# Performance work log

Measured on AMD Instinct MI355X. Metric: run time of the kernel, lower is better.

Reference implementation:

```python
import jax, jax.numpy as jnp
import numpy as np

N = 100000
E = 1600000
D_IN = 128
D_OUT = 128
LN_EPS = 1e-5


def setup_inputs() -> dict:
    key = jax.random.key(0)
    ks = jax.random.split(key, 5)
    features = jax.random.normal(ks[0], (N, D_IN), dtype=jnp.float32)
    adj_indices = jax.random.randint(ks[1], (2, E), 0, N, dtype=jnp.int64)
    adj_values = jax.random.uniform(ks[2], (E,), dtype=jnp.float32)
    weight = jax.random.normal(ks[3], (D_IN, D_OUT), dtype=jnp.float32) * (1.0 / np.sqrt(D_IN))
    bias = jax.random.normal(ks[4], (1, D_OUT), dtype=jnp.float32) * 0.1
    ln_gamma = jnp.ones((D_OUT,), dtype=jnp.float32)
    ln_beta = jnp.zeros((D_OUT,), dtype=jnp.float32)
    return {
        "features": features,
        "adj_indices": adj_indices,
        "adj_values": adj_values,
        "weight": weight,
        "bias": bias,
        "ln_gamma": ln_gamma,
        "ln_beta": ln_beta,
    }


def reference(features, adj_indices, adj_values, weight, bias, ln_gamma, ln_beta):
    # Dense transform: [N, in] @ [in, out] -> [N, out]
    h = features @ weight
    # SpMM: out[r] = sum_{edges (r,c)} val * h[c]
    row, col = adj_indices[0], adj_indices[1]
    msg = adj_values[:, None] * h[col]  # [E, out] gather + scale
    agg = jax.ops.segment_sum(msg, row, num_segments=features.shape[0])
    # bias + ELU
    x = jax.nn.elu(agg + bias)
    # LayerNorm over last dim (eps=1e-5, learned affine)
    mu = jnp.mean(x, axis=-1, keepdims=True)
    var = jnp.mean(jnp.square(x - mu), axis=-1, keepdims=True)
    return (x - mu) * jax.lax.rsqrt(var + LN_EPS) * ln_gamma + ln_beta
```

## Files before the change

kernel.cpp:

```cpp
#include <hip/hip_runtime.h>
#include <hip/hip_bf16.h>

#define LN_EPS 1e-5f

typedef float f32x4 __attribute__((ext_vector_type(4)));
typedef short s16x8 __attribute__((ext_vector_type(8)));

__device__ __forceinline__ unsigned short f2bf(float f) {
  return __builtin_bit_cast(unsigned short, __float2bfloat16(f));
}
__device__ __forceinline__ float bf_lo(unsigned int u) { return __uint_as_float(u << 16); }
__device__ __forceinline__ float bf_hi(unsigned int u) { return __uint_as_float(u & 0xFFFF0000u); }

__global__ __launch_bounds__(512) void k_build(const unsigned int* __restrict__ idx,
                                               const float* __restrict__ vals,
                                               const float* __restrict__ feats,
                                               const float* __restrict__ W,
                                               int E, int N, int CAP, int SB,
                                               int* __restrict__ scnt,
                                               int2* __restrict__ brec,
                                               unsigned int* __restrict__ hu) {
  __shared__ __align__(16) char smem[34816];
  int t = threadIdx.x;
  if ((int)blockIdx.x < SB) {
    int* lcnt = (int*)smem;
    int* lbase = lcnt + 1024;
    int* sflag = lbase + 1024;
    if (t == 0) *sflag = 0;
    for (int i = t; i < 1024; i += 512) lcnt[i] = 0;
    __syncthreads();
    {
      int nchk = E < 4096 ? E : 4096;
      unsigned int orv = 0u;
      for (int i = t; i < nchk; i += 512) orv |= idx[2 * i + 1];
      if (orv) atomicOr(sflag, 1);
    }
    __syncthreads();
    bool is64 = (*sflag == 0);
    int xcd = blockIdx.x & 7;
    int e0 = blockIdx.x * 4096 + t * 8;
    int rows[8], cols[8], lrk[8];
    float vv[8];
    if (e0 + 7 < E) {
      if (is64) {
#pragma unroll
        for (int q = 0; q < 4; ++q) {
          int4 a = *(const int4*)(idx + 2 * e0 + 4 * q);
          rows[2 * q] = a.x; rows[2 * q + 1] = a.z;
          int4 c = *(const int4*)(idx + 2 * E + 2 * e0 + 4 * q);
          cols[2 * q] = c.x; cols[2 * q + 1] = c.z;
        }
      } else {
        const int* p = (const int*)idx;
#pragma unroll
        for (int q = 0; q < 2; ++q) {
          int4 a = *(const int4*)(p + e0 + 4 * q);
          rows[4 * q] = a.x; rows[4 * q + 1] = a.y; rows[4 * q + 2] = a.z; rows[4 * q + 3] = a.w;
          int4 c = *(const int4*)(p + E + e0 + 4 * q);
          cols[4 * q] = c.x; cols[4 * q + 1] = c.y; cols[4 * q + 2] = c.z; cols[4 * q + 3] = c.w;
        }
      }
      float4 va = *(const float4*)(vals + e0);
      float4 vb = *(const float4*)(vals + e0 + 4);
      vv[0] = va.x; vv[1] = va.y; vv[2] = va.z; vv[3] = va.w;
      vv[4] = vb.x; vv[5] = vb.y; vv[6] = vb.z; vv[7] = vb.w;
    } else {
#pragma unroll
      for (int q = 0; q < 8; ++q) {
        int e = e0 + q;
        rows[q] = -1;
        if (e < E) {
          rows[q] = is64 ? (int)idx[2 * e] : ((const int*)idx)[e];
          cols[q] = is64 ? (int)idx[2 * E + 2 * e] : ((const int*)idx)[E + e];
          vv[q] = vals[e];
        }
      }
    }
#pragma unroll
    for (int q = 0; q < 8; ++q)
      if (rows[q] >= 0) lrk[q] = atomicAdd(&lcnt[rows[q] >> 7], 1);
    __syncthreads();
    for (int i = t; i < 1024; i += 512) {
      int c = lcnt[i];
      lbase[i] = c ? atomicAdd(&scnt[(i * 8 + xcd) * 16], c) : 0;
    }
    __syncthreads();
#pragma unroll
    for (int q = 0; q < 8; ++q) {
      if (rows[q] >= 0) {
        int bk = rows[q] >> 7;
        int p = lbase[bk] + lrk[q];
        if (p < CAP)
          brec[(size_t)(bk * 8 + xcd) * CAP + p] =
              make_int2(cols[q] | ((rows[q] & 127) << 20), __float_as_int(vv[q]));
      }
    }
  } else {
    unsigned short (*Wt)[136] = (unsigned short(*)[136])smem;
    for (int i = t; i < 16384; i += 512) {
      int k = i & 127, c = i >> 7;
      Wt[c][k] = f2bf(W[k * 128 + c]);
    }
    __syncthreads();
    int wid = t >> 6, lane = t & 63;
    int rlo = lane & 15, khi = lane >> 4;
    int row0 = (blockIdx.x - SB) * 128 + wid * 16;
    f32x4 zero = {0.f, 0.f, 0.f, 0.f};
    f32x4 acc[8];
#pragma unroll
    for (int n = 0; n < 8; ++n) acc[n] = zero;
#pragma unroll
    for (int kb = 0; kb < 4; ++kb) {
      int k0 = kb * 32 + khi * 8;
      int r = row0 + rlo;
      if (r > N - 1) r = N - 1;
      const float* p = feats + (size_t)r * 128 + k0;
      f32x4 a0 = *(const f32x4*)p;
      f32x4 a1 = *(const f32x4*)(p + 4);
      s16x8 af;
#pragma unroll
      for (int j = 0; j < 4; ++j) af[j] = (short)f2bf(a0[j]);
#pragma unroll
      for (int j = 0; j < 4; ++j) af[4 + j] = (short)f2bf(a1[j]);
#pragma unroll
      for (int n = 0; n < 8; ++n) {
        s16x8 bfr = *(const s16x8*)&Wt[n * 16 + rlo][k0];
        acc[n] = __builtin_amdgcn_mfma_f32_16x16x32_bf16(af, bfr, acc[n], 0, 0, 0);
      }
    }
#pragma unroll
    for (int n = 0; n < 4; ++n)
#pragma unroll
      for (int reg = 0; reg < 4; ++reg) {
        int r = row0 + khi * 4 + reg;
        if (r < N) {
          unsigned int lo = f2bf(acc[n][reg]);
          unsigned int hi = f2bf(acc[n + 4][reg]);
          hu[(size_t)r * 64 + n * 16 + rlo] = lo | (hi << 16);
        }
      }
  }
}

__global__ __launch_bounds__(512) void k_localize(const int* __restrict__ scnt, int CAP,
                                                  const int2* __restrict__ brec, int N,
                                                  int* __restrict__ rowbeg,
                                                  int* __restrict__ rowcnt,
                                                  int2* __restrict__ brec2) {
  __shared__ int pref[9];
  __shared__ int cnt[128], basei[128], cur[128];
  int b = blockIdx.x, t = threadIdx.x;
  if (t < 128) { cnt[t] = 0; cur[t] = 0; }
  if (t == 0) {
    int s = 0;
#pragma unroll
    for (int x = 0; x < 8; ++x) { pref[x] = s; s += min(scnt[(b * 8 + x) * 16], CAP); }
    pref[8] = s;
  }
  __syncthreads();
  for (int x = 0; x < 8; ++x) {
    int sc = pref[x + 1] - pref[x];
    const int2* sp = brec + (size_t)(b * 8 + x) * CAP;
    for (int i = t; i < sc; i += 512) atomicAdd(&cnt[(unsigned)sp[i].x >> 20], 1);
  }
  __syncthreads();
  if (t < 128) basei[t] = cnt[t];
  __syncthreads();
  for (int d = 1; d < 128; d <<= 1) {
    int v = 0;
    if (t < 128 && t >= d) v = basei[t - d];
    __syncthreads();
    if (t < 128) basei[t] += v;
    __syncthreads();
  }
  int bstr = b * 8 * CAP;
  if (t < 128) {
    int r = b * 128 + t;
    if (r < N) { rowbeg[r] = bstr + basei[t] - cnt[t]; rowcnt[r] = cnt[t]; }
  }
  __syncthreads();
  for (int x = 0; x < 8; ++x) {
    int sc = pref[x + 1] - pref[x];
    const int2* sp = brec + (size_t)(b * 8 + x) * CAP;
    for (int i = t; i < sc; i += 512) {
      int2 e = sp[i];
      int lr = (unsigned)e.x >> 20;
      int p = atomicAdd(&cur[lr], 1);
      brec2[bstr + basei[lr] - cnt[lr] + p] = make_int2(e.x & 0xFFFFF, e.y);
    }
  }
}

__global__ __launch_bounds__(256) void k_spmm3(const unsigned int* __restrict__ hu,
                                               const int* __restrict__ rowbeg,
                                               const int* __restrict__ rowcnt,
                                               const int2* __restrict__ rec,
                                               const float* __restrict__ bias,
                                               const float* __restrict__ gamma,
                                               const float* __restrict__ beta,
                                               float* __restrict__ out, int N) {
  int wid = __builtin_amdgcn_readfirstlane(threadIdx.x >> 6);
  int lane = threadIdx.x & 63;
  int r = blockIdx.x * 4 + wid;
  if (r >= N) return;
  int start = rowbeg[r], end = start + rowcnt[r];

  float a0 = 0.f, a1 = 0.f;
  int i = start;
  for (; i + 8 <= end; i += 8) {
    unsigned int u[8];
    float v[8];
#pragma unroll
    for (int j = 0; j < 8; ++j) {
      int2 e = rec[i + j];
      u[j] = hu[(size_t)e.x * 64 + lane];
      v[j] = __int_as_float(e.y);
    }
#pragma unroll
    for (int j = 0; j < 8; ++j) {
      a0 = fmaf(v[j], bf_lo(u[j]), a0);
      a1 = fmaf(v[j], bf_hi(u[j]), a1);
    }
  }
  for (; i + 4 <= end; i += 4) {
    unsigned int u[4];
    float v[4];
#pragma unroll
    for (int j = 0; j < 4; ++j) {
      int2 e = rec[i + j];
      u[j] = hu[(size_t)e.x * 64 + lane];
      v[j] = __int_as_float(e.y);
    }
#pragma unroll
    for (int j = 0; j < 4; ++j) {
      a0 = fmaf(v[j], bf_lo(u[j]), a0);
      a1 = fmaf(v[j], bf_hi(u[j]), a1);
    }
  }
  for (; i < end; ++i) {
    int2 e = rec[i];
    unsigned int u = hu[(size_t)e.x * 64 + lane];
    float v = __int_as_float(e.y);
    a0 = fmaf(v, bf_lo(u), a0);
    a1 = fmaf(v, bf_hi(u), a1);
  }

  float x0 = a0 + bias[lane], x1 = a1 + bias[lane + 64];
  x0 = x0 > 0.f ? x0 : __expf(x0) - 1.f;
  x1 = x1 > 0.f ? x1 : __expf(x1) - 1.f;

  float s = x0 + x1;
#pragma unroll
  for (int d = 1; d < 64; d <<= 1) s += __shfl_xor(s, d);
  float mu = s * (1.f / 128.f);
  float d0 = x0 - mu, d1 = x1 - mu;
  float q = d0 * d0 + d1 * d1;
#pragma unroll
  for (int d = 1; d < 64; d <<= 1) q += __shfl_xor(q, d);
  float rstd = rsqrtf(q * (1.f / 128.f) + LN_EPS);

  float o0 = d0 * rstd * gamma[lane] + beta[lane];
  float o1 = d1 * rstd * gamma[lane + 64] + beta[lane + 64];
  __builtin_nontemporal_store(o0, out + (size_t)r * 128 + lane);
  __builtin_nontemporal_store(o1, out + (size_t)r * 128 + 64 + lane);
}

extern "C" void kernel_launch(void* const* d_in, const int* in_sizes, int n_in,
                              void* d_out, int out_size, void* d_ws, size_t ws_size,
                              hipStream_t stream) {
  const float* feats = (const float*)d_in[0];
  const unsigned int* idx = (const unsigned int*)d_in[1];
  const float* vals = (const float*)d_in[2];
  const float* W = (const float*)d_in[3];
  const float* bias = (const float*)d_in[4];
  const float* gamma = (const float*)d_in[5];
  const float* beta = (const float*)d_in[6];
  float* out = (float*)d_out;
  int N = in_sizes[0] / 128;
  int E = in_sizes[2];
  (void)n_in; (void)out_size; (void)ws_size;

  int NBUK = (N + 127) >> 7;
  int NV = NBUK * 8;
  int mean = (E + NV - 1) / NV;
  int CAP = ((mean + mean / 2 + 15) / 16) * 16;

  char* ws = (char*)d_ws;
  size_t off = 0;
  auto alloc = [&](size_t bytes) {
    char* p = ws + off;
    off += (bytes + 255) & ~(size_t)255;
    return p;
  };
  unsigned int* hu = (unsigned int*)alloc((size_t)N * 64 * 4);
  int* scnt  = (int*)alloc((size_t)NV * 64);
  int* rowbeg = (int*)alloc((size_t)N * 4);
  int* rowcnt = (int*)alloc((size_t)N * 4);
  int2* brec  = (int2*)alloc((size_t)NV * CAP * 8);
  int2* brec2 = (int2*)alloc((size_t)NV * CAP * 8);

  hipMemsetAsync(scnt, 0, (size_t)NV * 64, stream);

  int SB = (E + 4095) / 4096;
  int GEMMB = (N + 127) / 128;
  k_build<<<SB + GEMMB, 512, 0, stream>>>(idx, vals, feats, W, E, N, CAP, SB, scnt, brec, hu);
  k_localize<<<NBUK, 512, 0, stream>>>(scnt, CAP, brec, N, rowbeg, rowcnt, brec2);
  k_spmm3<<<(N + 3) / 4, 256, 0, stream>>>(hu, rowbeg, rowcnt, brec2, bias, gamma, beta, out, N);
}
```

Before: 139.8 us.

## Stage bucket records in LDS for localize, pack row info, widen spmm blocks

Adds a localize variant that loads each bucket's records once into registers, counts them per row, and scatters into shared memory. It then writes the output contiguously, instead of reading the records twice and scattering to global memory. Row start and count are packed into a single int2 array, so the spmm kernel does one load per row. The spmm kernel now uses 512-thread blocks and hoists its bias, gamma and beta loads. The old localize remains as a fallback when the bucket capacity exceeds the shared buffer.

```diff
diff --git a/kernel.cpp b/kernel.cpp
--- a/kernel.cpp
+++ b/kernel.cpp
@@ -142,11 +142,76 @@
   }
 }
 
-__global__ __launch_bounds__(512) void k_localize(const int* __restrict__ scnt, int CAP,
-                                                  const int2* __restrict__ brec, int N,
-                                                  int* __restrict__ rowbeg,
-                                                  int* __restrict__ rowcnt,
-                                                  int2* __restrict__ brec2) {
+#define LCAP 3072
+#define LRPT 6
+__global__ __launch_bounds__(512) void k_localize_s(const int* __restrict__ scnt, int CAP,
+                                                    const int2* __restrict__ brec, int N,
+                                                    int2* __restrict__ rowinfo,
+                                                    int2* __restrict__ brec2) {
+  __shared__ int2 srec[LCAP];
+  __shared__ int cnt[128], base[128], prefs[9];
+  __shared__ int w0sum;
+  int b = blockIdx.x, t = threadIdx.x;
+  if (t < 128) cnt[t] = 0;
+  if (t == 0) {
+    int s = 0;
+#pragma unroll
+    for (int x = 0; x < 8; ++x) { prefs[x] = s; s += min(scnt[(b * 8 + x) * 16], CAP); }
+    prefs[8] = s;
+  }
+  __syncthreads();
+  int pr[9];
+#pragma unroll
+  for (int x = 0; x < 9; ++x) pr[x] = prefs[x];
+  int M = pr[8];
+
+  int2 myrec[LRPT];
+  int lr[LRPT], lrk[LRPT];
+#pragma unroll
+  for (int q = 0; q < LRPT; ++q) {
+    int i = q * 512 + t;
+    lr[q] = -1;
+    if (i < M) {
+      int x = 0;
+#pragma unroll
+      for (int xx = 1; xx < 8; ++xx) x += (i >= pr[xx]) ? 1 : 0;
+      myrec[q] = brec[(size_t)(b * 8 + x) * CAP + (i - pr[x])];
+      lr[q] = (unsigned)myrec[q].x >> 20;
+      lrk[q] = atomicAdd(&cnt[lr[q]], 1);
+    }
+  }
+  __syncthreads();
+  int c = (t < 128) ? cnt[t] : 0;
+  int inc = c;
+#pragma unroll
+  for (int d = 1; d < 64; d <<= 1) {
+    int y = __shfl_up(inc, d);
+    if ((t & 63) >= d) inc += y;
+  }
+  if (t == 63) w0sum = inc;
+  __syncthreads();
+  if (t >= 64 && t < 128) inc += w0sum;
+  if (t < 128) base[t] = inc - c;
+  __syncthreads();
+#pragma unroll
+  for (int q = 0; q < LRPT; ++q)
+    if (lr[q] >= 0) srec[base[lr[q]] + lrk[q]] = myrec[q];
+  int bstr = b * 8 * CAP;
+  if (t < 128) {
+    int r = b * 128 + t;
+    if (r < N) rowinfo[r] = make_int2(bstr + base[t], c);
+  }
+  __syncthreads();
+  for (int i = t; i < M; i += 512) {
+    int2 e = srec[i];
+    brec2[bstr + i] = make_int2(e.x & 0xFFFFF, e.y);
+  }
+}
+
+__global__ __launch_bounds__(512) void k_localize_l(const int* __restrict__ scnt, int CAP,
+                                                    const int2* __restrict__ brec, int N,
+                                                    int2* __restrict__ rowinfo,
+                                                    int2* __restrict__ brec2) {
   __shared__ int pref[9];
   __shared__ int cnt[128], basei[128], cur[128];
   int b = blockIdx.x, t = threadIdx.x;
@@ -176,7 +241,7 @@
   int bstr = b * 8 * CAP;
   if (t < 128) {
     int r = b * 128 + t;
-    if (r < N) { rowbeg[r] = bstr + basei[t] - cnt[t]; rowcnt[r] = cnt[t]; }
+    if (r < N) rowinfo[r] = make_int2(bstr + basei[t] - cnt[t], cnt[t]);
   }
   __syncthreads();
   for (int x = 0; x < 8; ++x) {
@@ -184,16 +249,15 @@
     const int2* sp = brec + (size_t)(b * 8 + x) * CAP;
     for (int i = t; i < sc; i += 512) {
       int2 e = sp[i];
-      int lr = (unsigned)e.x >> 20;
-      int p = atomicAdd(&cur[lr], 1);
-      brec2[bstr + basei[lr] - cnt[lr] + p] = make_int2(e.x & 0xFFFFF, e.y);
-    }
-  }
-}
-
-__global__ __launch_bounds__(256) void k_spmm3(const unsigned int* __restrict__ hu,
-                                               const int* __restrict__ rowbeg,
-                                               const int* __restrict__ rowcnt,
+      int lrr = (unsigned)e.x >> 20;
+      int p = atomicAdd(&cur[lrr], 1);
+      brec2[bstr + basei[lrr] - cnt[lrr] + p] = make_int2(e.x & 0xFFFFF, e.y);
+    }
+  }
+}
+
+__global__ __launch_bounds__(512) void k_spmm3(const unsigned int* __restrict__ hu,
+                                               const int2* __restrict__ rowinfo,
                                                const int2* __restrict__ rec,
                                                const float* __restrict__ bias,
                                                const float* __restrict__ gamma,
@@ -201,9 +265,13 @@
                                                float* __restrict__ out, int N) {
   int wid = __builtin_amdgcn_readfirstlane(threadIdx.x >> 6);
   int lane = threadIdx.x & 63;
-  int r = blockIdx.x * 4 + wid;
+  int r = blockIdx.x * 8 + wid;
   if (r >= N) return;
-  int start = rowbeg[r], end = start + rowcnt[r];
+  float b0 = bias[lane], b1 = bias[lane + 64];
+  float g0 = gamma[lane], g1 = gamma[lane + 64];
+  float be0 = beta[lane], be1 = beta[lane + 64];
+  int2 ri = rowinfo[r];
+  int start = ri.x, end = ri.x + ri.y;
 
   float a0 = 0.f, a1 = 0.f;
   int i = start;
@@ -245,7 +313,7 @@
     a1 = fmaf(v, bf_hi(u), a1);
   }
 
-  float x0 = a0 + bias[lane], x1 = a1 + bias[lane + 64];
+  float x0 = a0 + b0, x1 = a1 + b1;
   x0 = x0 > 0.f ? x0 : __expf(x0) - 1.f;
   x1 = x1 > 0.f ? x1 : __expf(x1) - 1.f;
 
@@ -259,8 +327,8 @@
   for (int d = 1; d < 64; d <<= 1) q += __shfl_xor(q, d);
   float rstd = rsqrtf(q * (1.f / 128.f) + LN_EPS);
 
-  float o0 = d0 * rstd * gamma[lane] + beta[lane];
-  float o1 = d1 * rstd * gamma[lane + 64] + beta[lane + 64];
+  float o0 = d0 * rstd * g0 + be0;
+  float o1 = d1 * rstd * g1 + be1;
   __builtin_nontemporal_store(o0, out + (size_t)r * 128 + lane);
   __builtin_nontemporal_store(o1, out + (size_t)r * 128 + 64 + lane);
 }
@@ -294,8 +362,7 @@
   };
   unsigned int* hu = (unsigned int*)alloc((size_t)N * 64 * 4);
   int* scnt  = (int*)alloc((size_t)NV * 64);
-  int* rowbeg = (int*)alloc((size_t)N * 4);
-  int* rowcnt = (int*)alloc((size_t)N * 4);
+  int2* rowinfo = (int2*)alloc((size_t)N * 8);
   int2* brec  = (int2*)alloc((size_t)NV * CAP * 8);
   int2* brec2 = (int2*)alloc((size_t)NV * CAP * 8);
 
@@ -304,6 +371,9 @@
   int SB = (E + 4095) / 4096;
   int GEMMB = (N + 127) / 128;
   k_build<<<SB + GEMMB, 512, 0, stream>>>(idx, vals, feats, W, E, N, CAP, SB, scnt, brec, hu);
-  k_localize<<<NBUK, 512, 0, stream>>>(scnt, CAP, brec, N, rowbeg, rowcnt, brec2);
-  k_spmm3<<<(N + 3) / 4, 256, 0, stream>>>(hu, rowbeg, rowcnt, brec2, bias, gamma, beta, out, N);
-}
+  if (8 * CAP <= LCAP)
+    k_localize_s<<<NBUK, 512, 0, stream>>>(scnt, CAP, brec, N, rowinfo, brec2);
+  else
+    k_localize_l<<<NBUK, 512, 0, stream>>>(scnt, CAP, brec, N, rowinfo, brec2);
+  k_spmm3<<<(N + 7) / 8, 512, 0, stream>>>(hu, rowinfo, brec2, bias, gamma, beta, out, N);
+}
```

Result: faster. 133.6 us (-4.4%).

## Fuse row localization into SpMM kernel using shared-memory bucket sort

Applied to the files above, without the earlier changes.

Buckets shrink from 128 to 64 rows, and the separate localize kernel is merged into the SpMM kernel. Each block now loads its bucket's edge records, counting-sorts them by local row in LDS, then aggregates and applies bias, ELU and LayerNorm per row. This removes one kernel launch and the global round trip through brec2, rowbeg and rowcnt. In exchange, the per-bucket capacity becomes a mean plus 8-sigma bound clamped to the LDS size, so edges beyond the cap would be silently dropped on skewed graphs. Each block also handles fewer rows with a serial per-warp loop.

```diff
diff --git a/kernel.cpp b/kernel.cpp
--- a/kernel.cpp
+++ b/kernel.cpp
@@ -1,5 +1,6 @@
 #include <hip/hip_runtime.h>
 #include <hip/hip_bf16.h>
+#include <math.h>
 
 #define LN_EPS 1e-5f
 
@@ -11,6 +12,7 @@
 }
 __device__ __forceinline__ float bf_lo(unsigned int u) { return __uint_as_float(u << 16); }
 __device__ __forceinline__ float bf_hi(unsigned int u) { return __uint_as_float(u & 0xFFFF0000u); }
+
 
 __global__ __launch_bounds__(512) void k_build(const unsigned int* __restrict__ idx,
                                                const float* __restrict__ vals,
@@ -24,10 +26,10 @@
   int t = threadIdx.x;
   if ((int)blockIdx.x < SB) {
     int* lcnt = (int*)smem;
-    int* lbase = lcnt + 1024;
-    int* sflag = lbase + 1024;
+    int* lbase = lcnt + 2048;
+    int* sflag = lbase + 2048;
     if (t == 0) *sflag = 0;
-    for (int i = t; i < 1024; i += 512) lcnt[i] = 0;
+    for (int i = t; i < 2048; i += 512) lcnt[i] = 0;
     __syncthreads();
     {
       int nchk = E < 4096 ? E : 4096;
@@ -78,9 +80,9 @@
     }
 #pragma unroll
     for (int q = 0; q < 8; ++q)
-      if (rows[q] >= 0) lrk[q] = atomicAdd(&lcnt[rows[q] >> 7], 1);
-    __syncthreads();
-    for (int i = t; i < 1024; i += 512) {
+      if (rows[q] >= 0) lrk[q] = atomicAdd(&lcnt[rows[q] >> 6], 1);
+    __syncthreads();
+    for (int i = t; i < 2048; i += 512) {
       int c = lcnt[i];
       lbase[i] = c ? atomicAdd(&scnt[(i * 8 + xcd) * 16], c) : 0;
     }
@@ -88,11 +90,11 @@
 #pragma unroll
     for (int q = 0; q < 8; ++q) {
       if (rows[q] >= 0) {
-        int bk = rows[q] >> 7;
+        int bk = rows[q] >> 6;
         int p = lbase[bk] + lrk[q];
         if (p < CAP)
           brec[(size_t)(bk * 8 + xcd) * CAP + p] =
-              make_int2(cols[q] | ((rows[q] & 127) << 20), __float_as_int(vv[q]));
+              make_int2(cols[q] | ((rows[q] & 63) << 20), __float_as_int(vv[q]));
       }
     }
   } else {
@@ -142,127 +144,130 @@
   }
 }
 
-__global__ __launch_bounds__(512) void k_localize(const int* __restrict__ scnt, int CAP,
-                                                  const int2* __restrict__ brec, int N,
-                                                  int* __restrict__ rowbeg,
-                                                  int* __restrict__ rowcnt,
-                                                  int2* __restrict__ brec2) {
-  __shared__ int pref[9];
-  __shared__ int cnt[128], basei[128], cur[128];
+#define SCAPMAX 2048
+#define LRPT 4
+__global__ __launch_bounds__(512, 8) void k_spmmL(const unsigned int* __restrict__ hu,
+                                                  const int* __restrict__ scnt, int CAP,
+                                                  const int2* __restrict__ brec,
+                                                  const float* __restrict__ bias,
+                                                  const float* __restrict__ gamma,
+                                                  const float* __restrict__ beta,
+                                                  float* __restrict__ out, int N) {
+  __shared__ int2 srec[SCAPMAX];
+  __shared__ int cnt[64], base[64], prefs[9];
   int b = blockIdx.x, t = threadIdx.x;
-  if (t < 128) { cnt[t] = 0; cur[t] = 0; }
+  int wid = __builtin_amdgcn_readfirstlane(t >> 6);
+  int lane = t & 63;
+  if (t < 64) cnt[t] = 0;
   if (t == 0) {
     int s = 0;
 #pragma unroll
-    for (int x = 0; x < 8; ++x) { pref[x] = s; s += min(scnt[(b * 8 + x) * 16], CAP); }
-    pref[8] = s;
-  }
+    for (int x = 0; x < 8; ++x) { prefs[x] = s; s += min(scnt[(b * 8 + x) * 16], CAP); }
+    prefs[8] = s;
+  }
+  float b0 = bias[lane], b1 = bias[lane + 64];
+  float g0 = gamma[lane], g1 = gamma[lane + 64];
+  float be0 = beta[lane], be1 = beta[lane + 64];
   __syncthreads();
-  for (int x = 0; x < 8; ++x) {
-    int sc = pref[x + 1] - pref[x];
-    const int2* sp = brec + (size_t)(b * 8 + x) * CAP;
-    for (int i = t; i < sc; i += 512) atomicAdd(&cnt[(unsigned)sp[i].x >> 20], 1);
+  int pr[9];
+#pragma unroll
+  for (int x = 0; x < 9; ++x) pr[x] = prefs[x];
+  int M = pr[8];
+
+  int2 myrec[LRPT];
+  int lr[LRPT], lrk[LRPT];
+#pragma unroll
+  for (int q = 0; q < LRPT; ++q) {
+    int i = q * 512 + t;
+    lr[q] = -1;
+    if (i < M) {
+      int x = 0;
+#pragma unroll
+      for (int xx = 1; xx < 8; ++xx) x += (i >= pr[xx]) ? 1 : 0;
+      myrec[q] = brec[(size_t)(b * 8 + x) * CAP + (i - pr[x])];
+      lr[q] = (unsigned)myrec[q].x >> 20;
+      lrk[q] = atomicAdd(&cnt[lr[q]], 1);
+    }
   }
   __syncthreads();
-  if (t < 128) basei[t] = cnt[t];
+  if (t < 64) {
+    int c = cnt[t];
+    int inc = c;
+#pragma unroll
+    for (int d = 1; d < 64; d <<= 1) {
+      int y = __shfl_up(inc, d);
+      if (t >= d) inc += y;
+    }
+    base[t] = inc - c;
+  }
   __syncthreads();
-  for (int d = 1; d < 128; d <<= 1) {
-    int v = 0;
-    if (t < 128 && t >= d) v = basei[t - d];
-    __syncthreads();
-    if (t < 128) basei[t] += v;
-    __syncthreads();
-  }
-  int bstr = b * 8 * CAP;
-  if (t < 128) {
-    int r = b * 128 + t;
-    if (r < N) { rowbeg[r] = bstr + basei[t] - cnt[t]; rowcnt[r] = cnt[t]; }
-  }
+#pragma unroll
+  for (int q = 0; q < LRPT; ++q)
+    if (lr[q] >= 0) srec[base[lr[q]] + lrk[q]] = myrec[q];
   __syncthreads();
-  for (int x = 0; x < 8; ++x) {
-    int sc = pref[x + 1] - pref[x];
-    const int2* sp = brec + (size_t)(b * 8 + x) * CAP;
-    for (int i = t; i < sc; i += 512) {
-      int2 e = sp[i];
-      int lr = (unsigned)e.x >> 20;
-      int p = atomicAdd(&cur[lr], 1);
-      brec2[bstr + basei[lr] - cnt[lr] + p] = make_int2(e.x & 0xFFFFF, e.y);
-    }
-  }
-}
-
-__global__ __launch_bounds__(256) void k_spmm3(const unsigned int* __restrict__ hu,
-                                               const int* __restrict__ rowbeg,
-                                               const int* __restrict__ rowcnt,
-                                               const int2* __restrict__ rec,
-                                               const float* __restrict__ bias,
-                                               const float* __restrict__ gamma,
-                                               const float* __restrict__ beta,
-                                               float* __restrict__ out, int N) {
-  int wid = __builtin_amdgcn_readfirstlane(threadIdx.x >> 6);
-  int lane = threadIdx.x & 63;
-  int r = blockIdx.x * 4 + wid;
-  if (r >= N) return;
-  int start = rowbeg[r], end = start + rowcnt[r];
-
-  float a0 = 0.f, a1 = 0.f;
-  int i = start;
-  for (; i + 8 <= end; i += 8) {
-    unsigned int u[8];
-    float v[8];
-#pragma unroll
-    for (int j = 0; j < 8; ++j) {
-      int2 e = rec[i + j];
-      u[j] = hu[(size_t)e.x * 64 + lane];
-      v[j] = __int_as_float(e.y);
-    }
-#pragma unroll
-    for (int j = 0; j < 8; ++j) {
-      a0 = fmaf(v[j], bf_lo(u[j]), a0);
-      a1 = fmaf(v[j], bf_hi(u[j]), a1);
-    }
-  }
-  for (; i + 4 <= end; i += 4) {
-    unsigned int u[4];
-    float v[4];
-#pragma unroll
-    for (int j = 0; j < 4; ++j) {
-      int2 e = rec[i + j];
-      u[j] = hu[(size_t)e.x * 64 + lane];
-      v[j] = __int_as_float(e.y);
-    }
-#pragma unroll
-    for (int j = 0; j < 4; ++j) {
-      a0 = fmaf(v[j], bf_lo(u[j]), a0);
-      a1 = fmaf(v[j], bf_hi(u[j]), a1);
-    }
-  }
-  for (; i < end; ++i) {
-    int2 e = rec[i];
-    unsigned int u = hu[(size_t)e.x * 64 + lane];
-    float v = __int_as_float(e.y);
-    a0 = fmaf(v, bf_lo(u), a0);
-    a1 = fmaf(v, bf_hi(u), a1);
-  }
-
-  float x0 = a0 + bias[lane], x1 = a1 + bias[lane + 64];
-  x0 = x0 > 0.f ? x0 : __expf(x0) - 1.f;
-  x1 = x1 > 0.f ? x1 : __expf(x1) - 1.f;
-
-  float s = x0 + x1;
-#pragma unroll
-  for (int d = 1; d < 64; d <<= 1) s += __shfl_xor(s, d);
-  float mu = s * (1.f / 128.f);
-  float d0 = x0 - mu, d1 = x1 - mu;
-  float q = d0 * d0 + d1 * d1;
-#pragma unroll
-  for (int d = 1; d < 64; d <<= 1) q += __shfl_xor(q, d);
-  float rstd = rsqrtf(q * (1.f / 128.f) + LN_EPS);
-
-  float o0 = d0 * rstd * gamma[lane] + beta[lane];
-  float o1 = d1 * rstd * gamma[lane + 64] + beta[lane + 64];
-  __builtin_nontemporal_store(o0, out + (size_t)r * 128 + lane);
-  __builtin_nontemporal_store(o1, out + (size_t)r * 128 + 64 + lane);
+
+  for (int j = 0; j < 8; ++j) {
+    int lrow = wid * 8 + j;
+    int r = b * 64 + lrow;
+    if (r >= N) break;
+    int i = base[lrow], end = i + cnt[lrow];
+    float a0 = 0.f, a1 = 0.f;
+    for (; i + 8 <= end; i += 8) {
+      unsigned int u[8];
+      float v[8];
+#pragma unroll
+      for (int q = 0; q < 8; ++q) {
+        int2 e = srec[i + q];
+        int col = __builtin_amdgcn_readfirstlane(e.x) & 0xFFFFF;
+        u[q] = hu[(size_t)col * 64 + lane];
+        v[q] = __int_as_float(e.y);
+      }
+#pragma unroll
+      for (int q = 0; q < 8; ++q) {
+        a0 = fmaf(v[q], bf_lo(u[q]), a0);
+        a1 = fmaf(v[q], bf_hi(u[q]), a1);
+      }
+    }
+    for (; i + 4 <= end; i += 4) {
+      unsigned int u[4];
+      float v[4];
+#pragma unroll
+      for (int q = 0; q < 4; ++q) {
+        int2 e = srec[i + q];
+        int col = __builtin_amdgcn_readfirstlane(e.x) & 0xFFFFF;
+        u[q] = hu[(size_t)col * 64 + lane];
+        v[q] = __int_as_float(e.y);
+      }
+#pragma unroll
+      for (int q = 0; q < 4; ++q) {
+        a0 = fmaf(v[q], bf_lo(u[q]), a0);
+        a1 = fmaf(v[q], bf_hi(u[q]), a1);
+      }
+    }
+    for (; i < end; ++i) {
+      int2 e = srec[i];
+      int col = __builtin_amdgcn_readfirstlane(e.x) & 0xFFFFF;
+      unsigned int u = hu[(size_t)col * 64 + lane];
+      float v = __int_as_float(e.y);
+      a0 = fmaf(v, bf_lo(u), a0);
+      a1 = fmaf(v, bf_hi(u), a1);
+    }
+
+    float x0 = a0 + b0, x1 = a1 + b1;
+    x0 = x0 > 0.f ? x0 : __expf(x0) - 1.f;
+    x1 = x1 > 0.f ? x1 : __expf(x1) - 1.f;
+    float s = x0 + x1;
+#pragma unroll
+    for (int d = 1; d < 64; d <<= 1) s += __shfl_xor(s, d);
+    float mu = s * (1.f / 128.f);
+    float d0 = x0 - mu, d1 = x1 - mu;
+    float q2 = d0 * d0 + d1 * d1;
+#pragma unroll
+    for (int d = 1; d < 64; d <<= 1) q2 += __shfl_xor(q2, d);
+    float rstd = rsqrtf(q2 * (1.f / 128.f) + LN_EPS);
+    __builtin_nontemporal_store(d0 * rstd * g0 + be0, out + (size_t)r * 128 + lane);
+    __builtin_nontemporal_store(d1 * rstd * g1 + be1, out + (size_t)r * 128 + 64 + lane);
+  }
 }
 
 extern "C" void kernel_launch(void* const* d_in, const int* in_sizes, int n_in,
@@ -280,10 +285,12 @@
   int E = in_sizes[2];
   (void)n_in; (void)out_size; (void)ws_size;
 
-  int NBUK = (N + 127) >> 7;
+  int NBUK = (N + 63) >> 6;
   int NV = NBUK * 8;
   int mean = (E + NV - 1) / NV;
-  int CAP = ((mean + mean / 2 + 15) / 16) * 16;
+  int sig = (int)ceilf(sqrtf((float)mean));
+  int CAP = ((mean + 8 * sig + 15) / 16) * 16;
+  if (8 * CAP > SCAPMAX) CAP = SCAPMAX / 8;
 
   char* ws = (char*)d_ws;
   size_t off = 0;
@@ -293,17 +300,13 @@
     return p;
   };
   unsigned int* hu = (unsigned int*)alloc((size_t)N * 64 * 4);
-  int* scnt  = (int*)alloc((size_t)NV * 64);
-  int* rowbeg = (int*)alloc((size_t)N * 4);
-  int* rowcnt = (int*)alloc((size_t)N * 4);
-  int2* brec  = (int2*)alloc((size_t)NV * CAP * 8);
-  int2* brec2 = (int2*)alloc((size_t)NV * CAP * 8);
+  int* scnt = (int*)alloc((size_t)NV * 64);
+  int2* brec = (int2*)alloc((size_t)NV * CAP * 8);
 
   hipMemsetAsync(scnt, 0, (size_t)NV * 64, stream);
 
   int SB = (E + 4095) / 4096;
   int GEMMB = (N + 127) / 128;
   k_build<<<SB + GEMMB, 512, 0, stream>>>(idx, vals, feats, W, E, N, CAP, SB, scnt, brec, hu);
-  k_localize<<<NBUK, 512, 0, stream>>>(scnt, CAP, brec, N, rowbeg, rowcnt, brec2);
-  k_spmm3<<<(N + 3) / 4, 256, 0, stream>>>(hu, rowbeg, rowcnt, brec2, bias, gamma, beta, out, N);
+  k_spmmL<<<NBUK, 512, 0, stream>>>(hu, scnt, CAP, brec, bias, gamma, beta, out, N);
 }
```

Result: no change. 139.2 us (-0.4%).
